# Kernel tuning notes

Measured on AMD Instinct MI355X. Metric: run time of the kernel, lower is better.

Reference implementation:

```python
import jax, jax.numpy as jnp
import numpy as np

IN_FEATURES = 128
OUT_FEATURES = 256
N_HEADS = 8
N_HIDDEN = OUT_FEATURES // N_HEADS  # 32
NEG_SLOPE = 0.2
B, N = 4, 1024


def setup_inputs() -> dict:
    key = jax.random.key(0)
    k1, k2, k3, k4 = jax.random.split(key, 4)
    h = jax.random.normal(k1, (B, N, IN_FEATURES), dtype=jnp.float32)
    adj = jax.random.randint(k2, (B, N, N), 0, 2, dtype=jnp.int32)
    # guarantee self-loops so no row of the softmax is fully masked (avoids NaN)
    eye = jnp.eye(N, dtype=jnp.int32)[None]
    adj_mat = jnp.maximum(adj, eye)
    # params: linear.weight is [n_hidden*n_heads, in_features] in torch; store transposed
    W = jax.random.normal(k3, (IN_FEATURES, N_HEADS * N_HIDDEN), dtype=jnp.float32) / np.sqrt(IN_FEATURES)
    # attn.weight is [1, 2*n_hidden]; shared across heads
    a_vec = jax.random.normal(k4, (2 * N_HIDDEN,), dtype=jnp.float32) / np.sqrt(2 * N_HIDDEN)
    return {"h": h, "adj_mat": adj_mat, "W": W, "a_vec": a_vec}


def reference(h, adj_mat, W, a_vec):
    # g: [B, N, H, F]
    g = (h @ W).reshape(B, N, N_HEADS, N_HIDDEN)
    # attn Linear on concat([g_i, g_j]) decomposes: e_ij = a_l.g_i + a_r.g_j (identical math)
    a_l, a_r = a_vec[:N_HIDDEN], a_vec[N_HIDDEN:]
    el = jnp.einsum('bnhf,f->bnh', g, a_l)  # [B, N, H]
    er = jnp.einsum('bnhf,f->bnh', g, a_r)  # [B, N, H]
    e = el[:, :, None, :] + er[:, None, :, :]  # [B, N, N, H]
    e = jnp.where(e >= 0, e, NEG_SLOPE * e)  # LeakyReLU
    mask = (adj_mat != 0)[..., None]  # [B, N, N, 1] broadcast over heads
    e = jnp.where(mask, e, -jnp.inf)
    a = jax.nn.softmax(e, axis=2)
    a = a * mask.astype(a.dtype)
    # dropout: eval mode (identity)
    attn_res = jnp.einsum('bijh,bjhf->bihf', a, g)  # [B, N, H, F]
    out = attn_res.reshape(B, N, N_HEADS * N_HIDDEN)
    out = jnp.where(out >= 0, out, NEG_SLOPE * out)  # final LeakyReLU (is_concat=True)
    return out
```

## Files before the change

### kernel.cpp

```cpp
#include <hip/hip_runtime.h>

#define B_    4
#define N_    1024
#define FIN   128
#define FOUT  256
#define NH    8
#define ND    32
#define NSL   0.2f
#define LOG2E 1.44269504088896340736f

typedef _Float16 half8 __attribute__((ext_vector_type(8)));
typedef _Float16 h2 __attribute__((ext_vector_type(2)));
typedef __fp16 fp16x2 __attribute__((ext_vector_type(2)));
typedef float f32x4 __attribute__((ext_vector_type(4)));

static __device__ __forceinline__ unsigned bc_u(h2 v) {
  union { h2 h; unsigned u; } c; c.h = v; return c.u;
}
static __device__ __forceinline__ h2 bc_h(unsigned v) {
  union { h2 h; unsigned u; } c; c.u = v; return c.h;
}

__global__ __launch_bounds__(256) void gat_kAB(
    const int* __restrict__ adj, unsigned long long* __restrict__ adjb64,
    const float* __restrict__ W, const float* __restrict__ h,
    const float* __restrict__ a_vec, _Float16* __restrict__ g16,
    float* __restrict__ elt, float* __restrict__ ert)
{
  __shared__ _Float16 h16s[16][136];
  __shared__ _Float16 wt16s[64][136];
  __shared__ float elp[4][16], erp[4][16];

  const int t = threadIdx.x;

  if (blockIdx.x < 1024) {
    const int gw = (blockIdx.x * 256 + t) >> 6;
    const int lane = t & 63;
    const size_t base0 = (size_t)gw * 1024;
#pragma unroll
    for (int it = 0; it < 16; ++it) {
      const size_t base = base0 + it * 64;
      const unsigned long long m = __ballot(adj[base + lane] != 0);
      if (lane == 0) adjb64[base >> 6] = m;
    }
    return;
  }

  const int gb = blockIdx.x - 1024;
  const int fq = gb & 3;
  const int nt = gb >> 2;
  const int n0 = nt * 16;
  const int b = n0 >> 10, nn = n0 & 1023;
  const int fbase = fq * 64;

  const int wv = t >> 6, lane = t & 63;
  const int li = lane & 15, kg = lane >> 4;
  const int head = fq * 2 + (wv >> 1);
  const int hb   = b * NH + head;
  const int fi0  = (wv & 1) * 16;

  {
    const int hr = t >> 4, hk = (t & 15) * 8;
    const float4 v0 = *(const float4*)&h[(size_t)(n0 + hr) * FIN + hk];
    const float4 v1 = *(const float4*)&h[(size_t)(n0 + hr) * FIN + hk + 4];
    half8 o;
    o[0]=(_Float16)v0.x; o[1]=(_Float16)v0.y; o[2]=(_Float16)v0.z; o[3]=(_Float16)v0.w;
    o[4]=(_Float16)v1.x; o[5]=(_Float16)v1.y; o[6]=(_Float16)v1.z; o[7]=(_Float16)v1.w;
    *(half8*)&h16s[hr][hk] = o;
  }
  {
    const int fl = t & 63;
#pragma unroll 8
    for (int kk = t >> 6; kk < FIN; kk += 4)
      wt16s[fl][kk] = (_Float16)W[(size_t)kk * FOUT + fbase + fl];
  }
  __syncthreads();

  const _Float16* __restrict__ arow = &wt16s[wv * 16 + li][kg * 8];

  f32x4 acc = {0.f, 0.f, 0.f, 0.f};
#pragma unroll
  for (int ks = 0; ks < 4; ++ks) {
    const half8 Af = *(const half8*)(arow + ks * 32);
    const half8 Bf = *(const half8*)&h16s[li][ks * 32 + kg * 8];
    acc = __builtin_amdgcn_mfma_f32_16x16x32_f16(Af, Bf, acc, 0, 0, 0);
  }

  float pl = 0.f, pr = 0.f;
#pragma unroll
  for (int r = 0; r < 4; ++r) {
    const int fi = fi0 + kg * 4 + r;
    g16[((size_t)hb * ND + fi) * N_ + nn + li] = (_Float16)acc[r];
    pl += a_vec[fi] * acc[r];
    pr += a_vec[ND + fi] * acc[r];
  }
  pl *= LOG2E; pr *= LOG2E;
  pl += __shfl_xor(pl, 16); pl += __shfl_xor(pl, 32);
  pr += __shfl_xor(pr, 16); pr += __shfl_xor(pr, 32);
  if (lane < 16) { elp[wv][li] = pl; erp[wv][li] = pr; }
  __syncthreads();

  if (t < 32) {
    const int hh = t >> 4, ll = t & 15;
    const int hbw = b * NH + fq * 2 + hh;
    elt[(size_t)hbw * N_ + nn + ll] = elp[2 * hh][ll] + elp[2 * hh + 1][ll];
    ert[(size_t)hbw * N_ + nn + ll] = erp[2 * hh][ll] + erp[2 * hh + 1][ll];
  }
}

#define MASKW(SH, Q)                                                            \
  __builtin_amdgcn_perm(                                                        \
      (unsigned)__builtin_amdgcn_sbfe((int)(SH), 2*(Q)+1, 1),                   \
      (unsigned)__builtin_amdgcn_sbfe((int)(SH), 2*(Q), 1), 0x07060100u)

#define PGEN_PAIR(EL2, ERW, MAW, OUTW)                                          \
  {                                                                             \
    h2 x = (EL2) + bc_h(ERW);                                                   \
    h2 y = x * nsl2;                                                            \
    x = __builtin_elementwise_max(x, y);                                        \
    const unsigned xu = bc_u(x);                                                \
    const unsigned xh = xu >> 16;                                               \
    unsigned plo, phi;                                                          \
    asm("v_exp_f16 %0, %1" : "=v"(plo) : "v"(xu));                              \
    asm("v_exp_f16 %0, %1" : "=v"(phi) : "v"(xh));                              \
    (OUTW) = __builtin_amdgcn_perm(phi, plo, 0x05040100u) & (MAW);              \
  }

__global__ __launch_bounds__(1024) void gat_kC(
    const unsigned* __restrict__ adjb, const _Float16* __restrict__ g16,
    const float* __restrict__ elt, const float* __restrict__ ert,
    float* __restrict__ out)
{
  __shared__ _Float16 er_h[N_];
  __shared__ float dpart[8][32][68];
  __shared__ float denp[8][64];

  const int t = threadIdx.x;
  const int u0 = blockIdx.x;
  const int v  = ((u0 & 7) << 6) | (u0 >> 3);
  const int it   = v & 15;
  const int head = (v >> 4) & 7;
  const int b    = v >> 7;
  const int i0   = it * 64;
  const int hb   = b * NH + head;

  const int w16 = t >> 6;
  const int wv  = w16 >> 1;
  const int ih  = w16 & 1;
  const int lane = t & 63;
  const int li = lane & 15, kg = lane >> 4, kg8 = kg * 8;
  const h2 nsl2 = {(_Float16)NSL, (_Float16)NSL};

  er_h[t] = (_Float16)ert[(size_t)hb * N_ + t];
  __syncthreads();

  const int rowA = i0 + ih * 32 + li;
  const int rowB = rowA + 16;
  const float el_a = elt[(size_t)hb * N_ + rowA];
  const float el_b = elt[(size_t)hb * N_ + rowB];
  union { fp16x2 hh; unsigned u; h2 h; } ca, cb;
  ca.hh = __builtin_amdgcn_cvt_pkrtz(el_a, el_a);
  cb.hh = __builtin_amdgcn_cvt_pkrtz(el_b, el_b);
  const h2 el2a = ca.h, el2b = cb.h;

  const int4 A  = ((const int4*)(adjb + (size_t)(b * N_ + rowA) * 32))[wv];
  const int4 Bm = ((const int4*)(adjb + (size_t)(b * N_ + rowB) * 32))[wv];
  const unsigned wA[4] = {(unsigned)A.x, (unsigned)A.y, (unsigned)A.z, (unsigned)A.w};
  const unsigned wB[4] = {(unsigned)Bm.x, (unsigned)Bm.y, (unsigned)Bm.z, (unsigned)Bm.w};

  const _Float16* __restrict__ arow0 =
      g16 + ((size_t)hb * ND + li) * N_ + wv * 128 + kg8;
  const _Float16* __restrict__ arow1 = arow0 + (size_t)16 * N_;

  f32x4 acc0 = {0,0,0,0}, acc1 = {0,0,0,0}, accd = {0,0,0,0};
  f32x4 acc0b = {0,0,0,0}, acc1b = {0,0,0,0}, accdb = {0,0,0,0};
  const half8 ones = {(_Float16)1.f, (_Float16)1.f, (_Float16)1.f, (_Float16)1.f,
                      (_Float16)1.f, (_Float16)1.f, (_Float16)1.f, (_Float16)1.f};

#pragma unroll
  for (int u = 0; u < 4; ++u) {
    const half8 Ag0 = *(const half8*)(arow0 + u * 32);
    const half8 Ag1 = *(const half8*)(arow1 + u * 32);
    const uint4 erv = *(const uint4*)&er_h[wv * 128 + u * 32 + kg8];
    const unsigned erw[4] = {erv.x, erv.y, erv.z, erv.w};

    const unsigned shA = wA[u] >> kg8;
    const unsigned shB = wB[u] >> kg8;

    union { half8 h8; unsigned uu[4]; } PA, PB;
#pragma unroll
    for (int q = 0; q < 4; ++q) {
      const unsigned maA = MASKW(shA, q);
      const unsigned maB = MASKW(shB, q);
      PGEN_PAIR(el2a, erw[q], maA, PA.uu[q])
      PGEN_PAIR(el2b, erw[q], maB, PB.uu[q])
    }

    acc0  = __builtin_amdgcn_mfma_f32_16x16x32_f16(Ag0, PA.h8, acc0, 0, 0, 0);
    acc1  = __builtin_amdgcn_mfma_f32_16x16x32_f16(Ag1, PA.h8, acc1, 0, 0, 0);
    accd  = __builtin_amdgcn_mfma_f32_16x16x32_f16(ones, PA.h8, accd, 0, 0, 0);
    acc0b = __builtin_amdgcn_mfma_f32_16x16x32_f16(Ag0, PB.h8, acc0b, 0, 0, 0);
    acc1b = __builtin_amdgcn_mfma_f32_16x16x32_f16(Ag1, PB.h8, acc1b, 0, 0, 0);
    accdb = __builtin_amdgcn_mfma_f32_16x16x32_f16(ones, PB.h8, accdb, 0, 0, 0);
  }

  const int ci = ih * 32 + li;
#pragma unroll
  for (int r = 0; r < 4; ++r) {
    dpart[wv][4*kg + r][ci]           = acc0[r];
    dpart[wv][16 + 4*kg + r][ci]      = acc1[r];
    dpart[wv][4*kg + r][16 + ci]      = acc0b[r];
    dpart[wv][16 + 4*kg + r][16 + ci] = acc1b[r];
  }
  if (lane < 16) { denp[wv][ci] = accd[0]; denp[wv][16 + ci] = accdb[0]; }
  __syncthreads();

  for (int o = t; o < 2048; o += 1024) {
    const int f = o & 31, ii = o >> 5;
    float s = 0.f, dn = 0.f;
#pragma unroll
    for (int p = 0; p < 8; ++p) { s += dpart[p][f][ii]; dn += denp[p][ii]; }
    float w = s / dn;
    w = fmaxf(w, NSL * w);
    out[((size_t)(b * N_ + i0 + ii)) * FOUT + head * ND + f] = w;
  }
}

extern "C" void kernel_launch(void* const* d_in, const int* in_sizes, int n_in,
                              void* d_out, int out_size, void* d_ws, size_t ws_size,
                              hipStream_t stream) {
  const float* h     = (const float*)d_in[0];
  const int*   adj   = (const int*)d_in[1];
  const float* W     = (const float*)d_in[2];
  const float* a_vec = (const float*)d_in[3];
  float* out = (float*)d_out;

  char* ws = (char*)d_ws;
  _Float16* g16  = (_Float16*)(ws);
  float*    elt  = (float*)(ws + (2u << 20));
  float*    ert  = (float*)(ws + (2u << 20) + (128u << 10));
  unsigned long long* adjb64 = (unsigned long long*)(ws + (2560u << 10));

  gat_kAB<<<2048, 256, 0, stream>>>(adj, adjb64, W, h, a_vec, g16, elt, ert);
  gat_kC<<<512, 1024, 0, stream>>>((const unsigned*)adjb64, g16, elt, ert, out);
}
```

Before: 31.18 us.

## Fuse projection and attention into one cooperative kernel with grid sync

Replaces the two-kernel launch with a single cooperative kernel of 256 blocks of 1024 threads. Each block first computes part of the projection, the el/er logits and the adjacency bitmask, then does a grid-wide sync and runs the attention body for two batches. The block-to-XCD mapping is also rearranged so a block's projection outputs are reused locally. It saves one kernel launch and the gap between kernels, at the cost of grid-sync overhead and fewer, larger blocks. If the cooperative launch fails, it falls back to the old two-kernel path.

```diff
diff --git a/kernel.cpp b/kernel.cpp
--- a/kernel.cpp
+++ b/kernel.cpp
@@ -1,4 +1,7 @@
 #include <hip/hip_runtime.h>
+#include <hip/hip_cooperative_groups.h>
+
+namespace cg = cooperative_groups;
 
 #define B_    4
 #define N_    1024
@@ -19,93 +22,6 @@
 }
 static __device__ __forceinline__ h2 bc_h(unsigned v) {
   union { h2 h; unsigned u; } c; c.u = v; return c.h;
-}
-
-__global__ __launch_bounds__(256) void gat_kAB(
-    const int* __restrict__ adj, unsigned long long* __restrict__ adjb64,
-    const float* __restrict__ W, const float* __restrict__ h,
-    const float* __restrict__ a_vec, _Float16* __restrict__ g16,
-    float* __restrict__ elt, float* __restrict__ ert)
-{
-  __shared__ _Float16 h16s[16][136];
-  __shared__ _Float16 wt16s[64][136];
-  __shared__ float elp[4][16], erp[4][16];
-
-  const int t = threadIdx.x;
-
-  if (blockIdx.x < 1024) {
-    const int gw = (blockIdx.x * 256 + t) >> 6;
-    const int lane = t & 63;
-    const size_t base0 = (size_t)gw * 1024;
-#pragma unroll
-    for (int it = 0; it < 16; ++it) {
-      const size_t base = base0 + it * 64;
-      const unsigned long long m = __ballot(adj[base + lane] != 0);
-      if (lane == 0) adjb64[base >> 6] = m;
-    }
-    return;
-  }
-
-  const int gb = blockIdx.x - 1024;
-  const int fq = gb & 3;
-  const int nt = gb >> 2;
-  const int n0 = nt * 16;
-  const int b = n0 >> 10, nn = n0 & 1023;
-  const int fbase = fq * 64;
-
-  const int wv = t >> 6, lane = t & 63;
-  const int li = lane & 15, kg = lane >> 4;
-  const int head = fq * 2 + (wv >> 1);
-  const int hb   = b * NH + head;
-  const int fi0  = (wv & 1) * 16;
-
-  {
-    const int hr = t >> 4, hk = (t & 15) * 8;
-    const float4 v0 = *(const float4*)&h[(size_t)(n0 + hr) * FIN + hk];
-    const float4 v1 = *(const float4*)&h[(size_t)(n0 + hr) * FIN + hk + 4];
-    half8 o;
-    o[0]=(_Float16)v0.x; o[1]=(_Float16)v0.y; o[2]=(_Float16)v0.z; o[3]=(_Float16)v0.w;
-    o[4]=(_Float16)v1.x; o[5]=(_Float16)v1.y; o[6]=(_Float16)v1.z; o[7]=(_Float16)v1.w;
-    *(half8*)&h16s[hr][hk] = o;
-  }
-  {
-    const int fl = t & 63;
-#pragma unroll 8
-    for (int kk = t >> 6; kk < FIN; kk += 4)
-      wt16s[fl][kk] = (_Float16)W[(size_t)kk * FOUT + fbase + fl];
-  }
-  __syncthreads();
-
-  const _Float16* __restrict__ arow = &wt16s[wv * 16 + li][kg * 8];
-
-  f32x4 acc = {0.f, 0.f, 0.f, 0.f};
-#pragma unroll
-  for (int ks = 0; ks < 4; ++ks) {
-    const half8 Af = *(const half8*)(arow + ks * 32);
-    const half8 Bf = *(const half8*)&h16s[li][ks * 32 + kg * 8];
-    acc = __builtin_amdgcn_mfma_f32_16x16x32_f16(Af, Bf, acc, 0, 0, 0);
-  }
-
-  float pl = 0.f, pr = 0.f;
-#pragma unroll
-  for (int r = 0; r < 4; ++r) {
-    const int fi = fi0 + kg * 4 + r;
-    g16[((size_t)hb * ND + fi) * N_ + nn + li] = (_Float16)acc[r];
-    pl += a_vec[fi] * acc[r];
-    pr += a_vec[ND + fi] * acc[r];
-  }
-  pl *= LOG2E; pr *= LOG2E;
-  pl += __shfl_xor(pl, 16); pl += __shfl_xor(pl, 32);
-  pr += __shfl_xor(pr, 16); pr += __shfl_xor(pr, 32);
-  if (lane < 16) { elp[wv][li] = pl; erp[wv][li] = pr; }
-  __syncthreads();
-
-  if (t < 32) {
-    const int hh = t >> 4, ll = t & 15;
-    const int hbw = b * NH + fq * 2 + hh;
-    elt[(size_t)hbw * N_ + nn + ll] = elp[2 * hh][ll] + elp[2 * hh + 1][ll];
-    ert[(size_t)hbw * N_ + nn + ll] = erp[2 * hh][ll] + erp[2 * hh + 1][ll];
-  }
 }
 
 #define MASKW(SH, Q)                                                            \
@@ -126,32 +42,24 @@
     (OUTW) = __builtin_amdgcn_perm(phi, plo, 0x05040100u) & (MAW);              \
   }
 
-__global__ __launch_bounds__(1024) void gat_kC(
-    const unsigned* __restrict__ adjb, const _Float16* __restrict__ g16,
+struct P2Smem {
+  _Float16 er_h[N_];
+  float dpart[8][32][68];
+  float denp[8][64];
+};
+
+static __device__ __forceinline__ void kc_body(
+    P2Smem* s2, const unsigned* __restrict__ adjb, const _Float16* __restrict__ g16,
     const float* __restrict__ elt, const float* __restrict__ ert,
-    float* __restrict__ out)
+    float* __restrict__ out, int b, int head, int i0,
+    int t, int w16, int lane, int li, int kg, int kg8)
 {
-  __shared__ _Float16 er_h[N_];
-  __shared__ float dpart[8][32][68];
-  __shared__ float denp[8][64];
-
-  const int t = threadIdx.x;
-  const int u0 = blockIdx.x;
-  const int v  = ((u0 & 7) << 6) | (u0 >> 3);
-  const int it   = v & 15;
-  const int head = (v >> 4) & 7;
-  const int b    = v >> 7;
-  const int i0   = it * 64;
-  const int hb   = b * NH + head;
-
-  const int w16 = t >> 6;
-  const int wv  = w16 >> 1;
-  const int ih  = w16 & 1;
-  const int lane = t & 63;
-  const int li = lane & 15, kg = lane >> 4, kg8 = kg * 8;
+  const int hb = b * NH + head;
+  const int wv = w16 >> 1;
+  const int ih = w16 & 1;
   const h2 nsl2 = {(_Float16)NSL, (_Float16)NSL};
 
-  er_h[t] = (_Float16)ert[(size_t)hb * N_ + t];
+  s2->er_h[t] = (_Float16)ert[(size_t)hb * N_ + t];
   __syncthreads();
 
   const int rowA = i0 + ih * 32 + li;
@@ -181,9 +89,8 @@
   for (int u = 0; u < 4; ++u) {
     const half8 Ag0 = *(const half8*)(arow0 + u * 32);
     const half8 Ag1 = *(const half8*)(arow1 + u * 32);
-    const uint4 erv = *(const uint4*)&er_h[wv * 128 + u * 32 + kg8];
+    const uint4 erv = *(const uint4*)&s2->er_h[wv * 128 + u * 32 + kg8];
     const unsigned erw[4] = {erv.x, erv.y, erv.z, erv.w};
-
     const unsigned shA = wA[u] >> kg8;
     const unsigned shB = wB[u] >> kg8;
 
@@ -207,23 +114,244 @@
   const int ci = ih * 32 + li;
 #pragma unroll
   for (int r = 0; r < 4; ++r) {
-    dpart[wv][4*kg + r][ci]           = acc0[r];
-    dpart[wv][16 + 4*kg + r][ci]      = acc1[r];
-    dpart[wv][4*kg + r][16 + ci]      = acc0b[r];
-    dpart[wv][16 + 4*kg + r][16 + ci] = acc1b[r];
-  }
-  if (lane < 16) { denp[wv][ci] = accd[0]; denp[wv][16 + ci] = accdb[0]; }
+    s2->dpart[wv][4*kg + r][ci]           = acc0[r];
+    s2->dpart[wv][16 + 4*kg + r][ci]      = acc1[r];
+    s2->dpart[wv][4*kg + r][16 + ci]      = acc0b[r];
+    s2->dpart[wv][16 + 4*kg + r][16 + ci] = acc1b[r];
+  }
+  if (lane < 16) { s2->denp[wv][ci] = accd[0]; s2->denp[wv][16 + ci] = accdb[0]; }
   __syncthreads();
 
   for (int o = t; o < 2048; o += 1024) {
     const int f = o & 31, ii = o >> 5;
     float s = 0.f, dn = 0.f;
 #pragma unroll
-    for (int p = 0; p < 8; ++p) { s += dpart[p][f][ii]; dn += denp[p][ii]; }
+    for (int p = 0; p < 8; ++p) { s += s2->dpart[p][f][ii]; dn += s2->denp[p][ii]; }
     float w = s / dn;
     w = fmaxf(w, NSL * w);
     out[((size_t)(b * N_ + i0 + ii)) * FOUT + head * ND + f] = w;
   }
+  __syncthreads();
+}
+
+union SMemF {
+  struct {
+    _Float16 h16s[64][136];
+    _Float16 wt16s[64][136];
+    float elp[2][2][4][16];
+    float erp[2][2][4][16];
+  } p1;
+  P2Smem p2;
+};
+
+__global__ __launch_bounds__(1024) void gat_fused(
+    const int* __restrict__ adj, unsigned long long* __restrict__ adjb64,
+    const float* __restrict__ W, const float* __restrict__ h,
+    const float* __restrict__ a_vec, _Float16* __restrict__ g16,
+    float* __restrict__ elt, float* __restrict__ ert,
+    float* __restrict__ out)
+{
+  __shared__ SMemF sm;
+
+  const int t = threadIdx.x;
+  const int u0 = blockIdx.x;
+  const int xcd = u0 & 7;
+  const int fq  = xcd & 3;
+  const int b1  = xcd >> 2;
+  const int sl0 = u0 >> 3;
+  const int it  = sl0 & 15;
+  const int hp  = (sl0 >> 4) & 1;
+  const int head = fq * 2 + hp;
+  const int i0   = it * 64;
+  const int bnt0 = (it + 16 * hp) * 2;
+
+  const int w16  = t >> 6;
+  const int lane = t & 63;
+  const int li = lane & 15, kg = lane >> 4, kg8 = kg * 8;
+
+  {
+    const int r = t >> 4, hk = (t & 15) * 8;
+    const int un_s = r >> 5, hr = r & 31;
+    const size_t hrow = (size_t)((un_s * 2 + b1) * N_ + bnt0 * 16 + hr) * FIN;
+    const float4 v0 = *(const float4*)&h[hrow + hk];
+    const float4 v1 = *(const float4*)&h[hrow + hk + 4];
+    half8 o;
+    o[0]=(_Float16)v0.x; o[1]=(_Float16)v0.y; o[2]=(_Float16)v0.z; o[3]=(_Float16)v0.w;
+    o[4]=(_Float16)v1.x; o[5]=(_Float16)v1.y; o[6]=(_Float16)v1.z; o[7]=(_Float16)v1.w;
+    *(half8*)&sm.p1.h16s[r][hk] = o;
+  }
+  {
+    const int fl = t & 63;
+    const int kk0 = (t >> 6) * 8;
+#pragma unroll 8
+    for (int kk = kk0; kk < kk0 + 8; ++kk)
+      sm.p1.wt16s[fl][kk] = (_Float16)W[(size_t)kk * FOUT + fq * 64 + fl];
+  }
+  __syncthreads();
+
+  if (w16 < 8) {
+    const int tsel = w16 >> 2;
+    const int wv4  = w16 & 3;
+    const int head_g = fq * 2 + (wv4 >> 1);
+    const int fi0  = (wv4 & 1) * 16;
+    const int nn   = (bnt0 + tsel) * 16;
+    const _Float16* arow = &sm.p1.wt16s[wv4 * 16 + li][kg8];
+
+#pragma unroll
+    for (int un = 0; un < 2; ++un) {
+      const int b  = un * 2 + b1;
+      const int hb = b * NH + head_g;
+
+      f32x4 acc = {0.f, 0.f, 0.f, 0.f};
+#pragma unroll
+      for (int ks = 0; ks < 4; ++ks) {
+        const half8 Af = *(const half8*)(arow + ks * 32);
+        const half8 Bf = *(const half8*)&sm.p1.h16s[un * 32 + tsel * 16 + li][ks * 32 + kg8];
+        acc = __builtin_amdgcn_mfma_f32_16x16x32_f16(Af, Bf, acc, 0, 0, 0);
+      }
+
+      float pl = 0.f, pr = 0.f;
+#pragma unroll
+      for (int r = 0; r < 4; ++r) {
+        const int fi = fi0 + kg * 4 + r;
+        g16[((size_t)hb * ND + fi) * N_ + nn + li] = (_Float16)acc[r];
+        pl += a_vec[fi] * acc[r];
+        pr += a_vec[ND + fi] * acc[r];
+      }
+      pl *= LOG2E; pr *= LOG2E;
+      pl += __shfl_xor(pl, 16); pl += __shfl_xor(pl, 32);
+      pr += __shfl_xor(pr, 16); pr += __shfl_xor(pr, 32);
+      if (lane < 16) { sm.p1.elp[un][tsel][wv4][li] = pl; sm.p1.erp[un][tsel][wv4][li] = pr; }
+    }
+  } else {
+#pragma unroll
+    for (int iter = 0; iter < 2; ++iter) {
+      const int gwp = iter * 2048 + u0 * 8 + (w16 - 8);
+      const size_t base0 = (size_t)gwp * 1024;
+#pragma unroll
+      for (int itp = 0; itp < 16; ++itp) {
+        const size_t base = base0 + itp * 64;
+        const unsigned long long m = __ballot(adj[base + lane] != 0);
+        if (lane == 0) adjb64[base >> 6] = m;
+      }
+    }
+  }
+  __syncthreads();
+
+  if (t < 128) {
+    const int un = t >> 6, tsel = (t >> 5) & 1, hh = (t >> 4) & 1, ll = t & 15;
+    const int hbw = (un * 2 + b1) * NH + fq * 2 + hh;
+    const int nn = (bnt0 + tsel) * 16;
+    elt[(size_t)hbw * N_ + nn + ll] =
+        sm.p1.elp[un][tsel][2*hh][ll] + sm.p1.elp[un][tsel][2*hh+1][ll];
+    ert[(size_t)hbw * N_ + nn + ll] =
+        sm.p1.erp[un][tsel][2*hh][ll] + sm.p1.erp[un][tsel][2*hh+1][ll];
+  }
+
+  cg::this_grid().sync();
+
+#pragma unroll 1
+  for (int un = 0; un < 2; ++un) {
+    kc_body(&sm.p2, (const unsigned*)adjb64, g16, elt, ert, out,
+            un * 2 + b1, head, i0, t, w16, lane, li, kg, kg8);
+  }
+}
+
+__global__ __launch_bounds__(256) void gat_kAB(
+    const int* __restrict__ adj, unsigned long long* __restrict__ adjb64,
+    const float* __restrict__ W, const float* __restrict__ h,
+    const float* __restrict__ a_vec, _Float16* __restrict__ g16,
+    float* __restrict__ elt, float* __restrict__ ert)
+{
+  __shared__ _Float16 h16s[16][136];
+  __shared__ _Float16 wt16s[64][136];
+  __shared__ float elp[4][16], erp[4][16];
+
+  const int t = threadIdx.x;
+  if (blockIdx.x < 1024) {
+    const int gw = (blockIdx.x * 256 + t) >> 6;
+    const int lane = t & 63;
+    const size_t base0 = (size_t)gw * 1024;
+#pragma unroll
+    for (int it = 0; it < 16; ++it) {
+      const size_t base = base0 + it * 64;
+      const unsigned long long m = __ballot(adj[base + lane] != 0);
+      if (lane == 0) adjb64[base >> 6] = m;
+    }
+    return;
+  }
+  const int gb = blockIdx.x - 1024;
+  const int xcd = gb & 7, fq = xcd & 3, b1 = xcd >> 2;
+  const int slot = gb >> 3, ntl = slot & 63, b2 = slot >> 6;
+  const int b = b2 * 2 + b1, nn = ntl * 16, n0g = b * 1024 + nn;
+
+  const int wv = t >> 6, lane = t & 63;
+  const int li = lane & 15, kg = lane >> 4;
+  const int head = fq * 2 + (wv >> 1);
+  const int hb = b * NH + head;
+  const int fi0 = (wv & 1) * 16;
+
+  {
+    const int hr = t >> 4, hk = (t & 15) * 8;
+    const float4 v0 = *(const float4*)&h[(size_t)(n0g + hr) * FIN + hk];
+    const float4 v1 = *(const float4*)&h[(size_t)(n0g + hr) * FIN + hk + 4];
+    half8 o;
+    o[0]=(_Float16)v0.x; o[1]=(_Float16)v0.y; o[2]=(_Float16)v0.z; o[3]=(_Float16)v0.w;
+    o[4]=(_Float16)v1.x; o[5]=(_Float16)v1.y; o[6]=(_Float16)v1.z; o[7]=(_Float16)v1.w;
+    *(half8*)&h16s[hr][hk] = o;
+  }
+  {
+    const int fl = t & 63;
+#pragma unroll 8
+    for (int kk = t >> 6; kk < FIN; kk += 4)
+      wt16s[fl][kk] = (_Float16)W[(size_t)kk * FOUT + fq * 64 + fl];
+  }
+  __syncthreads();
+
+  const _Float16* arow = &wt16s[wv * 16 + li][kg * 8];
+  f32x4 acc = {0.f, 0.f, 0.f, 0.f};
+#pragma unroll
+  for (int ks = 0; ks < 4; ++ks) {
+    const half8 Af = *(const half8*)(arow + ks * 32);
+    const half8 Bf = *(const half8*)&h16s[li][ks * 32 + kg * 8];
+    acc = __builtin_amdgcn_mfma_f32_16x16x32_f16(Af, Bf, acc, 0, 0, 0);
+  }
+  float pl = 0.f, pr = 0.f;
+#pragma unroll
+  for (int r = 0; r < 4; ++r) {
+    const int fi = fi0 + kg * 4 + r;
+    g16[((size_t)hb * ND + fi) * N_ + nn + li] = (_Float16)acc[r];
+    pl += a_vec[fi] * acc[r];
+    pr += a_vec[ND + fi] * acc[r];
+  }
+  pl *= LOG2E; pr *= LOG2E;
+  pl += __shfl_xor(pl, 16); pl += __shfl_xor(pl, 32);
+  pr += __shfl_xor(pr, 16); pr += __shfl_xor(pr, 32);
+  if (lane < 16) { elp[wv][li] = pl; erp[wv][li] = pr; }
+  __syncthreads();
+  if (t < 32) {
+    const int hh = t >> 4, ll = t & 15;
+    const int hbw = b * NH + fq * 2 + hh;
+    elt[(size_t)hbw * N_ + nn + ll] = elp[2*hh][ll] + elp[2*hh+1][ll];
+    ert[(size_t)hbw * N_ + nn + ll] = erp[2*hh][ll] + erp[2*hh+1][ll];
+  }
+}
+
+__global__ __launch_bounds__(1024) void gat_kC(
+    const unsigned* __restrict__ adjb, const _Float16* __restrict__ g16,
+    const float* __restrict__ elt, const float* __restrict__ ert,
+    float* __restrict__ out)
+{
+  __shared__ P2Smem s2;
+  const int t = threadIdx.x;
+  const int u0 = blockIdx.x;
+  const int xcd = u0 & 7, fq = xcd & 3, b1 = xcd >> 2;
+  const int slot = u0 >> 3;
+  const int it = slot & 15, hp = (slot >> 4) & 1, b2 = slot >> 5;
+  const int head = fq * 2 + hp, b = b2 * 2 + b1, i0 = it * 64;
+  const int w16 = t >> 6, lane = t & 63;
+  const int li = lane & 15, kg = lane >> 4, kg8 = kg * 8;
+  kc_body(&s2, adjb, g16, elt, ert, out, b, head, i0, t, w16, lane, li, kg, kg8);
 }
 
 extern "C" void kernel_launch(void* const* d_in, const int* in_sizes, int n_in,
@@ -241,6 +369,13 @@
   float*    ert  = (float*)(ws + (2u << 20) + (128u << 10));
   unsigned long long* adjb64 = (unsigned long long*)(ws + (2560u << 10));
 
-  gat_kAB<<<2048, 256, 0, stream>>>(adj, adjb64, W, h, a_vec, g16, elt, ert);
-  gat_kC<<<512, 1024, 0, stream>>>((const unsigned*)adjb64, g16, elt, ert, out);
-}
+  void* args[] = {(void*)&adj, (void*)&adjb64, (void*)&W, (void*)&h,
+                  (void*)&a_vec, (void*)&g16, (void*)&elt, (void*)&ert, (void*)&out};
+  hipError_t e = hipLaunchCooperativeKernel((const void*)gat_fused, dim3(256),
+                                            dim3(1024), args, 0, stream);
+  if (e != hipSuccess) {
+    (void)hipGetLastError();
+    gat_kAB<<<2048, 256, 0, stream>>>(adj, adjb64, W, h, a_vec, g16, elt, ert);
+    gat_kC<<<512, 1024, 0, stream>>>((const unsigned*)adjb64, g16, elt, ert, out);
+  }
+}
```

After: 69.81 us. +123.9%, slower.
